# Optimization experiments

Hardware: AMD Instinct MI355X
Metric: run time of the kernel (lower is better)

## Reference

```python
import jax, jax.numpy as jnp
import numpy as np

EMBED_DIM = 768
NUM_HEADS = 12
HEAD_SIZE = EMBED_DIM // NUM_HEADS


def setup_inputs() -> dict:
    key = jax.random.key(0)
    ks = jax.random.split(key, 9)
    B, S, D = 4, 2048, EMBED_DIM
    scale = 1.0 / np.sqrt(D)
    x = jax.random.normal(ks[0], (B, S, D), dtype=jnp.float32)
    # Linear params (torch nn.Linear: y = x @ W.T + b); store W as [in, out] for einsum
    Wq = jax.random.normal(ks[1], (D, D), dtype=jnp.float32) * scale
    bq = jnp.zeros((D,), dtype=jnp.float32)
    Wk = jax.random.normal(ks[2], (D, D), dtype=jnp.float32) * scale
    bk = jnp.zeros((D,), dtype=jnp.float32)
    Wv = jax.random.normal(ks[3], (D, D), dtype=jnp.float32) * scale
    bv = jnp.zeros((D,), dtype=jnp.float32)
    Wo = jax.random.normal(ks[4], (D, D), dtype=jnp.float32) * scale
    bo = jnp.zeros((D,), dtype=jnp.float32)
    return {"x": x, "Wq": Wq, "bq": bq, "Wk": Wk, "bk": bk,
            "Wv": Wv, "bv": bv, "Wo": Wo, "bo": bo}


def reference(x, Wq, bq, Wk, bk, Wv, bv, Wo, bo):
    B, S, D = x.shape
    H, hs = NUM_HEADS, HEAD_SIZE
    scale = hs ** (-0.5)
    # Projections
    Q = (x @ Wq + bq).reshape(B, S, H, hs)
    K = (x @ Wk + bk).reshape(B, S, H, hs)
    V = (x @ Wv + bv).reshape(B, S, H, hs)
    # Batched attention over all heads (equivalent to the per-head loop:
    # torch view splits last dim into H contiguous chunks; concat of per-head
    # outputs along -1 restores the same layout)
    scores = jnp.einsum('bqhd,bkhd->bhqk', Q, K) * scale  # [B,H,S,S]
    attn = jax.nn.softmax(scores, axis=-1)
    out = jnp.einsum('bhqk,bkhd->bqhd', attn, V).reshape(B, S, D)
    # Output projection; dropout is identity in eval mode
    return out @ Wo + bo
```

## Files before the change

### kernel.cpp

```cpp
#include <hip/hip_runtime.h>

typedef unsigned short ushort_t;
typedef __bf16 bf16x8 __attribute__((ext_vector_type(8)));
typedef float floatx4 __attribute__((ext_vector_type(4)));

__device__ inline ushort_t f2bf(float f) {
    __bf16 h = (__bf16)f;
    return __builtin_bit_cast(ushort_t, h);
}

__device__ inline void gload16(const void* g, void* l) {
    __builtin_amdgcn_global_load_lds((const __attribute__((address_space(1))) void*)g,
                                     (__attribute__((address_space(3))) void*)l, 16, 0, 0);
}

__global__ __launch_bounds__(256) void cast_x_kernel(const float* __restrict__ x,
                                                     ushort_t* __restrict__ o) {
    int i = (blockIdx.x * 256 + threadIdx.x) * 4;
    float4 v = *(const float4*)(x + i);
    ushort4 u;
    u.x = f2bf(v.x); u.y = f2bf(v.y); u.z = f2bf(v.z); u.w = f2bf(v.w);
    *(ushort4*)(o + i) = u;
}

__global__ __launch_bounds__(256) void wt_kernel(const float* __restrict__ W0, const float* __restrict__ W1,
                                                 const float* __restrict__ W2, const float* __restrict__ W3,
                                                 ushort_t* __restrict__ T0, ushort_t* __restrict__ T1,
                                                 ushort_t* __restrict__ T2, ushort_t* __restrict__ T3) {
    __shared__ float t[32][33];
    const float* W; ushort_t* T;
    switch (blockIdx.z) {
        case 0: W = W0; T = T0; break;
        case 1: W = W1; T = T1; break;
        case 2: W = W2; T = T2; break;
        default: W = W3; T = T3; break;
    }
    int n0 = blockIdx.x * 32, k0 = blockIdx.y * 32;
    int tx = threadIdx.x, ty = threadIdx.y;
    for (int i = 0; i < 4; ++i)
        t[ty + i * 8][tx] = W[(k0 + ty + i * 8) * 768 + n0 + tx];
    __syncthreads();
    for (int i = 0; i < 4; ++i)
        T[(n0 + ty + i * 8) * 768 + k0 + tx] = f2bf(t[tx][ty + i * 8]);
}

__global__ __launch_bounds__(256) void gemm_qkv(
    const ushort_t* __restrict__ A,
    const ushort_t* __restrict__ Tq, const ushort_t* __restrict__ Tk, const ushort_t* __restrict__ Tv,
    const float* __restrict__ bq, const float* __restrict__ bk, const float* __restrict__ bv,
    ushort_t* __restrict__ Qb, ushort_t* __restrict__ Kb, ushort_t* __restrict__ Vtb) {
    __shared__ ushort_t As[128 * 64];
    __shared__ ushort_t Bs[128 * 64];
    int tid = threadIdx.x;
    int m0 = blockIdx.x * 128;
    int nt = blockIdx.y;
    int which = nt / 6;
    int n0 = (nt % 6) * 128;
    const ushort_t* Bt = which == 0 ? Tq : (which == 1 ? Tk : Tv);
    const float* bias = which == 0 ? bq : (which == 1 ? bk : bv);

    int wave = tid >> 6;
    int lane = tid & 63;
    int ln = tid & 15;
    int quad = (tid >> 4) & 3;
    int wm = (wave & 1) * 64;
    int wn = (wave >> 1) * 64;
    int lr = lane >> 3;
    int lc = (lane & 7) * 8;

    floatx4 acc[4][4];
    floatx4 z = {0.f, 0.f, 0.f, 0.f};
    for (int i = 0; i < 4; ++i)
        for (int j = 0; j < 4; ++j) acc[i][j] = z;

    for (int kt = 0; kt < 12; ++kt) {
        int k0 = kt * 64;
        __syncthreads();
        for (int i = 0; i < 4; ++i) {
            int c = wave * 4 + i;
            int row = c * 8 + lr;
            gload16(&A[(m0 + row) * 768 + k0 + lc], &As[c * 512]);
            gload16(&Bt[(n0 + row) * 768 + k0 + lc], &Bs[c * 512]);
        }
        __syncthreads();
        for (int ks = 0; ks < 2; ++ks) {
            bf16x8 a[4], b[4];
            for (int i = 0; i < 4; ++i)
                a[i] = *(const bf16x8*)&As[(wm + i * 16 + ln) * 64 + ks * 32 + quad * 8];
            for (int j = 0; j < 4; ++j)
                b[j] = *(const bf16x8*)&Bs[(wn + j * 16 + ln) * 64 + ks * 32 + quad * 8];
            for (int i = 0; i < 4; ++i)
                for (int j = 0; j < 4; ++j)
                    acc[i][j] = __builtin_amdgcn_mfma_f32_16x16x32_bf16(a[i], b[j], acc[i][j], 0, 0, 0);
        }
    }

    const float QSCALE = 0.125f * 1.44269504088896f;
    for (int i = 0; i < 4; ++i) {
        for (int j = 0; j < 4; ++j) {
            int gn = n0 + wn + j * 16 + ln;
            float bia = bias[gn];
            int h = gn >> 6, dd = gn & 63;
            for (int r = 0; r < 4; ++r) {
                int gm = m0 + wm + i * 16 + quad * 4 + r;
                int bb = gm >> 11, ss = gm & 2047;
                float v = acc[i][j][r] + bia;
                if (which == 0) {
                    Qb[((bb * 12 + h) * 2048 + ss) * 64 + dd] = f2bf(v * QSCALE);
                } else if (which == 1) {
                    Kb[((bb * 12 + h) * 2048 + ss) * 64 + dd] = f2bf(v);
                } else {
                    Vtb[((bb * 12 + h) * 64 + dd) * 2048 + ss] = f2bf(v);
                }
            }
        }
    }
}

__global__ __launch_bounds__(256) void attn_kernel(
    const ushort_t* __restrict__ Qb, const ushort_t* __restrict__ Kb,
    const ushort_t* __restrict__ Vtb, ushort_t* __restrict__ Ob) {
    __shared__ ushort_t Ks[2][64 * 72];
    __shared__ ushort_t Vs[2][64 * 72];
    int tid = threadIdx.x;
    int qt = blockIdx.x;
    int bh = blockIdx.y;
    int wave = tid >> 6;
    int ln = tid & 15;
    int quad = (tid >> 4) & 3;
    int q0 = qt * 128 + wave * 32;

    const ushort_t* Qp = Qb + (size_t)bh * 2048 * 64;
    const ushort_t* Kp = Kb + (size_t)bh * 2048 * 64;
    const ushort_t* Vp = Vtb + (size_t)bh * 64 * 2048;

    bf16x8 bqf[2][2];
    for (int g = 0; g < 2; ++g)
        for (int ks = 0; ks < 2; ++ks)
            bqf[g][ks] = *(const bf16x8*)&Qp[(q0 + g * 16 + ln) * 64 + ks * 32 + quad * 8];

    int srow = tid >> 3;
    int c8 = tid & 7;
    int scol = c8 * 8;
    int u = c8 & 3;
    int vcol = (c8 >> 2) * 32 + (u & 1) * 16 + (u >> 1) * 4;

    uint4 kreg[2], vreg[2];

    for (int p = 0; p < 2; ++p) {
        kreg[p] = *(const uint4*)&Kp[(p * 32 + srow) * 64 + scol];
        vreg[p] = *(const uint4*)&Vp[(p * 32 + srow) * 2048 + scol];
    }
    for (int p = 0; p < 2; ++p) {
        *(uint4*)&Ks[0][(p * 32 + srow) * 72 + scol] = kreg[p];
        ushort_t* vb = &Vs[0][(p * 32 + srow) * 72 + vcol];
        *(uint2*)vb = make_uint2(vreg[p].x, vreg[p].y);
        *(uint2*)(vb + 8) = make_uint2(vreg[p].z, vreg[p].w);
    }
    __syncthreads();

    floatx4 o_acc[2][4];
    float lsum[2] = {0.f, 0.f};
    floatx4 z = {0.f, 0.f, 0.f, 0.f};
    for (int g = 0; g < 2; ++g)
        for (int m4 = 0; m4 < 4; ++m4) o_acc[g][m4] = z;

    for (int kt = 0; kt < 32; ++kt) {
        int cur = kt & 1;
        if (kt < 31) {
            for (int p = 0; p < 2; ++p) {
                kreg[p] = *(const uint4*)&Kp[((kt + 1) * 64 + p * 32 + srow) * 64 + scol];
                vreg[p] = *(const uint4*)&Vp[(p * 32 + srow) * 2048 + (kt + 1) * 64 + scol];
            }
        }

        const ushort_t* KsH = Ks[cur];
        const ushort_t* VsH = Vs[cur];

        bf16x8 ak[4][2];
        for (int m4 = 0; m4 < 4; ++m4)
            for (int ks = 0; ks < 2; ++ks)
                ak[m4][ks] = *(const bf16x8*)&KsH[(m4 * 16 + ln) * 72 + ks * 32 + quad * 8];

        floatx4 st[2][4];
        for (int g = 0; g < 2; ++g)
            for (int m4 = 0; m4 < 4; ++m4) {
                floatx4 s = z;
                s = __builtin_amdgcn_mfma_f32_16x16x32_bf16(ak[m4][0], bqf[g][0], s, 0, 0, 0);
                s = __builtin_amdgcn_mfma_f32_16x16x32_bf16(ak[m4][1], bqf[g][1], s, 0, 0, 0);
                st[g][m4] = s;
            }

        float pv[2][4][4];
        for (int g = 0; g < 2; ++g)
            for (int m4 = 0; m4 < 4; ++m4)
                for (int r = 0; r < 4; ++r) {
                    float e = __builtin_amdgcn_exp2f(st[g][m4][r]);
                    pv[g][m4][r] = e;
                    lsum[g] += e;
                }

        bf16x8 av[4][2];
        for (int m4 = 0; m4 < 4; ++m4)
            for (int c = 0; c < 2; ++c)
                av[m4][c] = *(const bf16x8*)&VsH[(m4 * 16 + ln) * 72 + c * 32 + quad * 8];

        for (int g = 0; g < 2; ++g) {
            bf16x8 bp[2];
            for (int c = 0; c < 2; ++c) {
                bf16x8 b;
                b[0] = (__bf16)pv[g][2 * c][0];
                b[1] = (__bf16)pv[g][2 * c][1];
                b[2] = (__bf16)pv[g][2 * c][2];
                b[3] = (__bf16)pv[g][2 * c][3];
                b[4] = (__bf16)pv[g][2 * c + 1][0];
                b[5] = (__bf16)pv[g][2 * c + 1][1];
                b[6] = (__bf16)pv[g][2 * c + 1][2];
                b[7] = (__bf16)pv[g][2 * c + 1][3];
                bp[c] = b;
            }
            for (int m4 = 0; m4 < 4; ++m4)
                for (int c = 0; c < 2; ++c)
                    o_acc[g][m4] = __builtin_amdgcn_mfma_f32_16x16x32_bf16(av[m4][c], bp[c], o_acc[g][m4], 0, 0, 0);
        }

        if (kt < 31) {
            int nxt = cur ^ 1;
            for (int p = 0; p < 2; ++p) {
                *(uint4*)&Ks[nxt][(p * 32 + srow) * 72 + scol] = kreg[p];
                ushort_t* vb = &Vs[nxt][(p * 32 + srow) * 72 + vcol];
                *(uint2*)vb = make_uint2(vreg[p].x, vreg[p].y);
                *(uint2*)(vb + 8) = make_uint2(vreg[p].z, vreg[p].w);
            }
        }
        __syncthreads();
    }

    for (int g = 0; g < 2; ++g) {
        lsum[g] += __shfl_xor(lsum[g], 16);
        lsum[g] += __shfl_xor(lsum[g], 32);
    }

    int b = bh / 12, h = bh % 12;
    for (int g = 0; g < 2; ++g) {
        float inv = 1.f / lsum[g];
        int token = b * 2048 + q0 + g * 16 + ln;
        for (int m4 = 0; m4 < 4; ++m4)
            for (int r = 0; r < 4; ++r)
                Ob[token * 768 + h * 64 + m4 * 16 + quad * 4 + r] = f2bf(o_acc[g][m4][r] * inv);
    }
}

__global__ __launch_bounds__(256) void gemm_out(
    const ushort_t* __restrict__ A, const ushort_t* __restrict__ Bt,
    const float* __restrict__ bias, float* __restrict__ out) {
    __shared__ ushort_t As[128 * 64];
    __shared__ ushort_t Bs[128 * 64];
    int tid = threadIdx.x;
    int m0 = blockIdx.x * 128;
    int n0 = blockIdx.y * 128;

    int wave = tid >> 6;
    int lane = tid & 63;
    int ln = tid & 15;
    int quad = (tid >> 4) & 3;
    int wm = (wave & 1) * 64;
    int wn = (wave >> 1) * 64;
    int lr = lane >> 3;
    int lc = (lane & 7) * 8;

    floatx4 acc[4][4];
    floatx4 z = {0.f, 0.f, 0.f, 0.f};
    for (int i = 0; i < 4; ++i)
        for (int j = 0; j < 4; ++j) acc[i][j] = z;

    for (int kt = 0; kt < 12; ++kt) {
        int k0 = kt * 64;
        __syncthreads();
        for (int i = 0; i < 4; ++i) {
            int c = wave * 4 + i;
            int row = c * 8 + lr;
            gload16(&A[(m0 + row) * 768 + k0 + lc], &As[c * 512]);
            gload16(&Bt[(n0 + row) * 768 + k0 + lc], &Bs[c * 512]);
        }
        __syncthreads();
        for (int ks = 0; ks < 2; ++ks) {
            bf16x8 a[4], b[4];
            for (int i = 0; i < 4; ++i)
                a[i] = *(const bf16x8*)&As[(wm + i * 16 + ln) * 64 + ks * 32 + quad * 8];
            for (int j = 0; j < 4; ++j)
                b[j] = *(const bf16x8*)&Bs[(wn + j * 16 + ln) * 64 + ks * 32 + quad * 8];
            for (int i = 0; i < 4; ++i)
                for (int j = 0; j < 4; ++j)
                    acc[i][j] = __builtin_amdgcn_mfma_f32_16x16x32_bf16(a[i], b[j], acc[i][j], 0, 0, 0);
        }
    }

    for (int i = 0; i < 4; ++i) {
        for (int j = 0; j < 4; ++j) {
            int gn = n0 + wn + j * 16 + ln;
            float bia = bias[gn];
            for (int r = 0; r < 4; ++r) {
                int gm = m0 + wm + i * 16 + quad * 4 + r;
                out[gm * 768 + gn] = acc[i][j][r] + bia;
            }
        }
    }
}

extern "C" void kernel_launch(void* const* d_in, const int* in_sizes, int n_in,
                              void* d_out, int out_size, void* d_ws, size_t ws_size,
                              hipStream_t stream) {
    const float* x  = (const float*)d_in[0];
    const float* Wq = (const float*)d_in[1];
    const float* bq = (const float*)d_in[2];
    const float* Wk = (const float*)d_in[3];
    const float* bk = (const float*)d_in[4];
    const float* Wv = (const float*)d_in[5];
    const float* bv = (const float*)d_in[6];
    const float* Wo = (const float*)d_in[7];
    const float* bo = (const float*)d_in[8];

    const int NTOK = 4 * 2048;
    const int NELT = NTOK * 768;
    const int WELT = 768 * 768;

    ushort_t* xbf = (ushort_t*)d_ws;
    ushort_t* Tq  = xbf + NELT;
    ushort_t* Tk  = Tq + WELT;
    ushort_t* Tv  = Tk + WELT;
    ushort_t* To  = Tv + WELT;
    ushort_t* Qb  = To + WELT;
    ushort_t* Kb  = Qb + NELT;
    ushort_t* Vtb = Kb + NELT;
    ushort_t* Ob  = Vtb + NELT;

    cast_x_kernel<<<NELT / 1024, 256, 0, stream>>>(x, xbf);
    wt_kernel<<<dim3(24, 24, 4), dim3(32, 8), 0, stream>>>(Wq, Wk, Wv, Wo, Tq, Tk, Tv, To);
    gemm_qkv<<<dim3(64, 18), 256, 0, stream>>>(xbf, Tq, Tk, Tv, bq, bk, bv, Qb, Kb, Vtb);
    attn_kernel<<<dim3(16, 48), 256, 0, stream>>>(Qb, Kb, Vtb, Ob);
    gemm_out<<<dim3(64, 6), 256, 0, stream>>>(Ob, To, bo, (float*)d_out);
}
```

Baseline: 235.3 us.

## Double-buffer GEMM tiles, fuse prep kernels, compute softmax row sums via MFMA

Both GEMMs switch from direct global-to-LDS loads with two barriers per k-step to register-prefetched, padded, double-buffered LDS tiles with one barrier per step, to overlap loads with MFMA and reduce bank conflicts. The cast and weight-transpose kernels are merged into one launch to save launch overhead. In attention, the per-lane exp accumulation and cross-lane shuffle reduction are replaced by an MFMA against a ones vector, so row sums now use the bf16-rounded probabilities. This doubles LDS usage in the GEMMs, which may lower occupancy.

```diff
diff --git a/kernel.cpp b/kernel.cpp
--- a/kernel.cpp
+++ b/kernel.cpp
@@ -9,39 +9,38 @@
     return __builtin_bit_cast(ushort_t, h);
 }
 
-__device__ inline void gload16(const void* g, void* l) {
-    __builtin_amdgcn_global_load_lds((const __attribute__((address_space(1))) void*)g,
-                                     (__attribute__((address_space(3))) void*)l, 16, 0, 0);
-}
-
-__global__ __launch_bounds__(256) void cast_x_kernel(const float* __restrict__ x,
-                                                     ushort_t* __restrict__ o) {
-    int i = (blockIdx.x * 256 + threadIdx.x) * 4;
-    float4 v = *(const float4*)(x + i);
-    ushort4 u;
-    u.x = f2bf(v.x); u.y = f2bf(v.y); u.z = f2bf(v.z); u.w = f2bf(v.w);
-    *(ushort4*)(o + i) = u;
-}
-
-__global__ __launch_bounds__(256) void wt_kernel(const float* __restrict__ W0, const float* __restrict__ W1,
-                                                 const float* __restrict__ W2, const float* __restrict__ W3,
-                                                 ushort_t* __restrict__ T0, ushort_t* __restrict__ T1,
-                                                 ushort_t* __restrict__ T2, ushort_t* __restrict__ T3) {
-    __shared__ float t[32][33];
-    const float* W; ushort_t* T;
-    switch (blockIdx.z) {
-        case 0: W = W0; T = T0; break;
-        case 1: W = W1; T = T1; break;
-        case 2: W = W2; T = T2; break;
-        default: W = W3; T = T3; break;
-    }
-    int n0 = blockIdx.x * 32, k0 = blockIdx.y * 32;
-    int tx = threadIdx.x, ty = threadIdx.y;
-    for (int i = 0; i < 4; ++i)
-        t[ty + i * 8][tx] = W[(k0 + ty + i * 8) * 768 + n0 + tx];
-    __syncthreads();
-    for (int i = 0; i < 4; ++i)
-        T[(n0 + ty + i * 8) * 768 + k0 + tx] = f2bf(t[tx][ty + i * 8]);
+__global__ __launch_bounds__(256) void prep_kernel(
+    const float* __restrict__ x, ushort_t* __restrict__ xbf,
+    const float* __restrict__ W0, const float* __restrict__ W1,
+    const float* __restrict__ W2, const float* __restrict__ W3,
+    ushort_t* __restrict__ T0, ushort_t* __restrict__ T1,
+    ushort_t* __restrict__ T2, ushort_t* __restrict__ T3) {
+    int bx = blockIdx.x;
+    int tid = threadIdx.x;
+    if (bx < 2304) {
+        __shared__ float t[32][33];
+        int w = bx / 576, rem = bx % 576;
+        const float* W; ushort_t* T;
+        switch (w) {
+            case 0: W = W0; T = T0; break;
+            case 1: W = W1; T = T1; break;
+            case 2: W = W2; T = T2; break;
+            default: W = W3; T = T3; break;
+        }
+        int n0 = (rem / 24) * 32, k0 = (rem % 24) * 32;
+        int tx = tid & 31, ty = tid >> 5;
+        for (int i = 0; i < 4; ++i)
+            t[ty + i * 8][tx] = W[(k0 + ty + i * 8) * 768 + n0 + tx];
+        __syncthreads();
+        for (int i = 0; i < 4; ++i)
+            T[(n0 + ty + i * 8) * 768 + k0 + tx] = f2bf(t[tx][ty + i * 8]);
+    } else {
+        int i = ((bx - 2304) * 256 + tid) * 4;
+        float4 v = *(const float4*)(x + i);
+        ushort4 u;
+        u.x = f2bf(v.x); u.y = f2bf(v.y); u.z = f2bf(v.z); u.w = f2bf(v.w);
+        *(ushort4*)(xbf + i) = u;
+    }
 }
 
 __global__ __launch_bounds__(256) void gemm_qkv(
@@ -49,8 +48,8 @@
     const ushort_t* __restrict__ Tq, const ushort_t* __restrict__ Tk, const ushort_t* __restrict__ Tv,
     const float* __restrict__ bq, const float* __restrict__ bk, const float* __restrict__ bv,
     ushort_t* __restrict__ Qb, ushort_t* __restrict__ Kb, ushort_t* __restrict__ Vtb) {
-    __shared__ ushort_t As[128 * 64];
-    __shared__ ushort_t Bs[128 * 64];
+    __shared__ ushort_t As[2][128 * 72];
+    __shared__ ushort_t Bs[2][128 * 72];
     int tid = threadIdx.x;
     int m0 = blockIdx.x * 128;
     int nt = blockIdx.y;
@@ -60,39 +59,61 @@
     const float* bias = which == 0 ? bq : (which == 1 ? bk : bv);
 
     int wave = tid >> 6;
-    int lane = tid & 63;
     int ln = tid & 15;
     int quad = (tid >> 4) & 3;
     int wm = (wave & 1) * 64;
     int wn = (wave >> 1) * 64;
-    int lr = lane >> 3;
-    int lc = (lane & 7) * 8;
 
     floatx4 acc[4][4];
     floatx4 z = {0.f, 0.f, 0.f, 0.f};
     for (int i = 0; i < 4; ++i)
         for (int j = 0; j < 4; ++j) acc[i][j] = z;
 
+    int srow = tid >> 3;
+    int scol = (tid & 7) * 8;
+
+    uint4 ar[4], br[4];
+    for (int p = 0; p < 4; ++p) {
+        int r = p * 32 + srow;
+        ar[p] = *(const uint4*)&A[(m0 + r) * 768 + scol];
+        br[p] = *(const uint4*)&Bt[(n0 + r) * 768 + scol];
+    }
+    for (int p = 0; p < 4; ++p) {
+        int r = p * 32 + srow;
+        *(uint4*)&As[0][r * 72 + scol] = ar[p];
+        *(uint4*)&Bs[0][r * 72 + scol] = br[p];
+    }
+    __syncthreads();
+
     for (int kt = 0; kt < 12; ++kt) {
-        int k0 = kt * 64;
-        __syncthreads();
-        for (int i = 0; i < 4; ++i) {
-            int c = wave * 4 + i;
-            int row = c * 8 + lr;
-            gload16(&A[(m0 + row) * 768 + k0 + lc], &As[c * 512]);
-            gload16(&Bt[(n0 + row) * 768 + k0 + lc], &Bs[c * 512]);
-        }
-        __syncthreads();
+        int cur = kt & 1;
+        if (kt < 11) {
+            int k0 = (kt + 1) * 64;
+            for (int p = 0; p < 4; ++p) {
+                int r = p * 32 + srow;
+                ar[p] = *(const uint4*)&A[(m0 + r) * 768 + k0 + scol];
+                br[p] = *(const uint4*)&Bt[(n0 + r) * 768 + k0 + scol];
+            }
+        }
         for (int ks = 0; ks < 2; ++ks) {
             bf16x8 a[4], b[4];
             for (int i = 0; i < 4; ++i)
-                a[i] = *(const bf16x8*)&As[(wm + i * 16 + ln) * 64 + ks * 32 + quad * 8];
+                a[i] = *(const bf16x8*)&As[cur][(wm + i * 16 + ln) * 72 + ks * 32 + quad * 8];
             for (int j = 0; j < 4; ++j)
-                b[j] = *(const bf16x8*)&Bs[(wn + j * 16 + ln) * 64 + ks * 32 + quad * 8];
+                b[j] = *(const bf16x8*)&Bs[cur][(wn + j * 16 + ln) * 72 + ks * 32 + quad * 8];
             for (int i = 0; i < 4; ++i)
                 for (int j = 0; j < 4; ++j)
                     acc[i][j] = __builtin_amdgcn_mfma_f32_16x16x32_bf16(a[i], b[j], acc[i][j], 0, 0, 0);
         }
+        if (kt < 11) {
+            int nxt = cur ^ 1;
+            for (int p = 0; p < 4; ++p) {
+                int r = p * 32 + srow;
+                *(uint4*)&As[nxt][r * 72 + scol] = ar[p];
+                *(uint4*)&Bs[nxt][r * 72 + scol] = br[p];
+            }
+        }
+        __syncthreads();
     }
 
     const float QSCALE = 0.125f * 1.44269504088896f;
@@ -139,6 +160,9 @@
         for (int ks = 0; ks < 2; ++ks)
             bqf[g][ks] = *(const bf16x8*)&Qp[(q0 + g * 16 + ln) * 64 + ks * 32 + quad * 8];
 
+    bf16x8 ones;
+    for (int j = 0; j < 8; ++j) ones[j] = (__bf16)1.0f;
+
     int srow = tid >> 3;
     int c8 = tid & 7;
     int scol = c8 * 8;
@@ -160,10 +184,12 @@
     __syncthreads();
 
     floatx4 o_acc[2][4];
-    float lsum[2] = {0.f, 0.f};
+    floatx4 acc_l[2];
     floatx4 z = {0.f, 0.f, 0.f, 0.f};
-    for (int g = 0; g < 2; ++g)
+    for (int g = 0; g < 2; ++g) {
+        acc_l[g] = z;
         for (int m4 = 0; m4 < 4; ++m4) o_acc[g][m4] = z;
+    }
 
     for (int kt = 0; kt < 32; ++kt) {
         int cur = kt & 1;
@@ -191,15 +217,6 @@
                 st[g][m4] = s;
             }
 
-        float pv[2][4][4];
-        for (int g = 0; g < 2; ++g)
-            for (int m4 = 0; m4 < 4; ++m4)
-                for (int r = 0; r < 4; ++r) {
-                    float e = __builtin_amdgcn_exp2f(st[g][m4][r]);
-                    pv[g][m4][r] = e;
-                    lsum[g] += e;
-                }
-
         bf16x8 av[4][2];
         for (int m4 = 0; m4 < 4; ++m4)
             for (int c = 0; c < 2; ++c)
@@ -209,19 +226,18 @@
             bf16x8 bp[2];
             for (int c = 0; c < 2; ++c) {
                 bf16x8 b;
-                b[0] = (__bf16)pv[g][2 * c][0];
-                b[1] = (__bf16)pv[g][2 * c][1];
-                b[2] = (__bf16)pv[g][2 * c][2];
-                b[3] = (__bf16)pv[g][2 * c][3];
-                b[4] = (__bf16)pv[g][2 * c + 1][0];
-                b[5] = (__bf16)pv[g][2 * c + 1][1];
-                b[6] = (__bf16)pv[g][2 * c + 1][2];
-                b[7] = (__bf16)pv[g][2 * c + 1][3];
+                for (int j = 0; j < 8; ++j) {
+                    int m4 = 2 * c + (j >> 2);
+                    int r = j & 3;
+                    b[j] = (__bf16)__builtin_amdgcn_exp2f(st[g][m4][r]);
+                }
                 bp[c] = b;
             }
             for (int m4 = 0; m4 < 4; ++m4)
                 for (int c = 0; c < 2; ++c)
                     o_acc[g][m4] = __builtin_amdgcn_mfma_f32_16x16x32_bf16(av[m4][c], bp[c], o_acc[g][m4], 0, 0, 0);
+            for (int c = 0; c < 2; ++c)
+                acc_l[g] = __builtin_amdgcn_mfma_f32_16x16x32_bf16(ones, bp[c], acc_l[g], 0, 0, 0);
         }
 
         if (kt < 31) {
@@ -236,14 +252,9 @@
         __syncthreads();
     }
 
-    for (int g = 0; g < 2; ++g) {
-        lsum[g] += __shfl_xor(lsum[g], 16);
-        lsum[g] += __shfl_xor(lsum[g], 32);
-    }
-
     int b = bh / 12, h = bh % 12;
     for (int g = 0; g < 2; ++g) {
-        float inv = 1.f / lsum[g];
+        float inv = 1.f / acc_l[g][0];
         int token = b * 2048 + q0 + g * 16 + ln;
         for (int m4 = 0; m4 < 4; ++m4)
             for (int r = 0; r < 4; ++r)
@@ -254,46 +265,68 @@
 __global__ __launch_bounds__(256) void gemm_out(
     const ushort_t* __restrict__ A, const ushort_t* __restrict__ Bt,
     const float* __restrict__ bias, float* __restrict__ out) {
-    __shared__ ushort_t As[128 * 64];
-    __shared__ ushort_t Bs[128 * 64];
+    __shared__ ushort_t As[2][128 * 72];
+    __shared__ ushort_t Bs[2][128 * 72];
     int tid = threadIdx.x;
     int m0 = blockIdx.x * 128;
     int n0 = blockIdx.y * 128;
 
     int wave = tid >> 6;
-    int lane = tid & 63;
     int ln = tid & 15;
     int quad = (tid >> 4) & 3;
     int wm = (wave & 1) * 64;
     int wn = (wave >> 1) * 64;
-    int lr = lane >> 3;
-    int lc = (lane & 7) * 8;
 
     floatx4 acc[4][4];
     floatx4 z = {0.f, 0.f, 0.f, 0.f};
     for (int i = 0; i < 4; ++i)
         for (int j = 0; j < 4; ++j) acc[i][j] = z;
 
+    int srow = tid >> 3;
+    int scol = (tid & 7) * 8;
+
+    uint4 ar[4], br[4];
+    for (int p = 0; p < 4; ++p) {
+        int r = p * 32 + srow;
+        ar[p] = *(const uint4*)&A[(m0 + r) * 768 + scol];
+        br[p] = *(const uint4*)&Bt[(n0 + r) * 768 + scol];
+    }
+    for (int p = 0; p < 4; ++p) {
+        int r = p * 32 + srow;
+        *(uint4*)&As[0][r * 72 + scol] = ar[p];
+        *(uint4*)&Bs[0][r * 72 + scol] = br[p];
+    }
+    __syncthreads();
+
     for (int kt = 0; kt < 12; ++kt) {
-        int k0 = kt * 64;
-        __syncthreads();
-        for (int i = 0; i < 4; ++i) {
-            int c = wave * 4 + i;
-            int row = c * 8 + lr;
-            gload16(&A[(m0 + row) * 768 + k0 + lc], &As[c * 512]);
-            gload16(&Bt[(n0 + row) * 768 + k0 + lc], &Bs[c * 512]);
-        }
-        __syncthreads();
+        int cur = kt & 1;
+        if (kt < 11) {
+            int k0 = (kt + 1) * 64;
+            for (int p = 0; p < 4; ++p) {
+                int r = p * 32 + srow;
+                ar[p] = *(const uint4*)&A[(m0 + r) * 768 + k0 + scol];
+                br[p] = *(const uint4*)&Bt[(n0 + r) * 768 + k0 + scol];
+            }
+        }
         for (int ks = 0; ks < 2; ++ks) {
             bf16x8 a[4], b[4];
             for (int i = 0; i < 4; ++i)
-                a[i] = *(const bf16x8*)&As[(wm + i * 16 + ln) * 64 + ks * 32 + quad * 8];
+                a[i] = *(const bf16x8*)&As[cur][(wm + i * 16 + ln) * 72 + ks * 32 + quad * 8];
             for (int j = 0; j < 4; ++j)
-                b[j] = *(const bf16x8*)&Bs[(wn + j * 16 + ln) * 64 + ks * 32 + quad * 8];
+                b[j] = *(const bf16x8*)&Bs[cur][(wn + j * 16 + ln) * 72 + ks * 32 + quad * 8];
             for (int i = 0; i < 4; ++i)
                 for (int j = 0; j < 4; ++j)
                     acc[i][j] = __builtin_amdgcn_mfma_f32_16x16x32_bf16(a[i], b[j], acc[i][j], 0, 0, 0);
         }
+        if (kt < 11) {
+            int nxt = cur ^ 1;
+            for (int p = 0; p < 4; ++p) {
+                int r = p * 32 + srow;
+                *(uint4*)&As[nxt][r * 72 + scol] = ar[p];
+                *(uint4*)&Bs[nxt][r * 72 + scol] = br[p];
+            }
+        }
+        __syncthreads();
     }
 
     for (int i = 0; i < 4; ++i) {
@@ -335,8 +368,7 @@
     ushort_t* Vtb = Kb + NELT;
     ushort_t* Ob  = Vtb + NELT;
 
-    cast_x_kernel<<<NELT / 1024, 256, 0, stream>>>(x, xbf);
-    wt_kernel<<<dim3(24, 24, 4), dim3(32, 8), 0, stream>>>(Wq, Wk, Wv, Wo, Tq, Tk, Tv, To);
+    prep_kernel<<<8448, 256, 0, stream>>>(x, xbf, Wq, Wk, Wv, Wo, Tq, Tk, Tv, To);
     gemm_qkv<<<dim3(64, 18), 256, 0, stream>>>(xbf, Tq, Tk, Tv, bq, bk, bv, Qb, Kb, Vtb);
     attn_kernel<<<dim3(16, 48), 256, 0, stream>>>(Qb, Kb, Vtb, Ob);
     gemm_out<<<dim3(64, 6), 256, 0, stream>>>(Ob, To, bo, (float*)d_out);
```

New measurement: 242.8 us. 1.03x slower.
